# Kernel tuning notes

Hardware: AMD Instinct MI355X
Metric: run time of the kernel (lower is better)

## Reference

```python
import jax, jax.numpy as jnp
import numpy as np

WORD_TOTAL = 1_000_000
POS_TOTAL = 123
DIM = 50        # word embedding dim
DWPE = 5        # position embedding dim
C = 230         # conv filters (dimensionC)
WIN = 3         # conv window
REL = 53        # relationTotal
B = 1024        # bag size (number of sentences)
L = 128         # sentence length


def setup_inputs() -> dict:
    key = jax.random.key(0)
    ks = jax.random.split(key, 12)
    con = np.sqrt(6.0 / (C + REL))
    con1 = np.sqrt(6.0 / ((DWPE + DIM) * WIN))
    inp = {
        "sen": jax.random.randint(ks[0], (B, L), 0, WORD_TOTAL),
        "p1": jax.random.randint(ks[1], (B, L), 0, POS_TOTAL),
        "p2": jax.random.randint(ks[2], (B, L), 0, POS_TOTAL),
        "wordVec": jax.random.normal(ks[3], (WORD_TOTAL, DIM), jnp.float32) * 0.05,
        "posVec1": jax.random.normal(ks[4], (POS_TOTAL, DWPE), jnp.float32) * con1,
        "posVec2": jax.random.normal(ks[5], (POS_TOTAL, DWPE), jnp.float32) * con1,
        "Wv": jax.random.normal(ks[6], (WIN, DIM, C), jnp.float32) * 0.05,
        "Wp1": jax.random.normal(ks[7], (WIN, DWPE, C), jnp.float32) * 0.05,
        "Wp2": jax.random.normal(ks[8], (WIN, DWPE, C), jnp.float32) * 0.05,
        "bv": jnp.zeros((C,), jnp.float32),
        "bp1": jnp.zeros((C,), jnp.float32),
        "bp2": jnp.zeros((C,), jnp.float32),
        "attW": jax.random.normal(ks[9], (C, C), jnp.float32) * con,
        "MR": jax.random.normal(ks[10], (C, REL), jnp.float32) * 0.05,
        "MRb": jnp.zeros((REL,), jnp.float32),
        "rel": 7,
    }
    return inp


def _conv_full_width(emb, W):
    Lout = emb.shape[1] - WIN + 1
    wins = jnp.stack([emb[:, j:j + Lout, :] for j in range(WIN)], axis=0)
    return jnp.einsum('jbld,jdc->blc', wins, W)  # [B, Lout, C]


def reference(sen, p1, p2, wordVec, posVec1, posVec2, Wv, bv, Wp1, bp1, Wp2, bp2, attW, MR, MRb, rel):
    # ---- encode: per-sentence PCNN-style encoder, batched over the bag ----
    ev = wordVec[sen]   # [B, L, DIM]
    e1 = posVec1[p1]    # [B, L, DWPE]
    e2 = posVec2[p2]    # [B, L, DWPE]
    c = (_conv_full_width(ev, Wv) + bv
         + _conv_full_width(e1, Wp1) + bp1
         + _conv_full_width(e2, Wp2) + bp2)          # [B, Lout, C]
    cnn_output = jnp.tanh(jnp.max(c, axis=1))          # [B, C]
    # ---- selective attention over the bag (training=False: dropout identity) ----
    scores = (cnn_output @ attW) @ MR + MRb            # [B, REL]
    weight = jax.nn.softmax(scores[:, rel])            # [B] = exp/sum(exp)
    att_output = jnp.sum(weight[:, None] * cnn_output, axis=0)[None, :]  # [1, C]
    output = jax.nn.softmax(att_output @ MR + MRb)     # [1, REL]
    return (output, att_output, cnn_output, weight[:, None])
```

## Files before the change

kernel.cpp:

```cpp
#include <hip/hip_runtime.h>
#include <math.h>

#define CCH 230
#define REL 53
#define BAG 1024
#define SLEN 128
#define LOUT 126

typedef __bf16 bf16x8 __attribute__((ext_vector_type(8)));
typedef float f32x4 __attribute__((ext_vector_type(4)));

#define WS_BF_USHORTS (16 * 6 * 64 * 8)
#define WS_BSUM 24576
#define WS_V    24832
#define WS_SCORES 25088

__device__ __forceinline__ unsigned short f2bf(float f) {
    unsigned u = __builtin_bit_cast(unsigned, f);
    unsigned r = (u + 0x7fffu + ((u >> 16) & 1u)) >> 16;
    return (unsigned short)r;
}

__global__ void pa_kernel(const float* __restrict__ Wv, const float* __restrict__ Wp1,
                          const float* __restrict__ Wp2, const float* __restrict__ bv,
                          const float* __restrict__ bp1, const float* __restrict__ bp2,
                          const float* __restrict__ attW, const float* __restrict__ MR,
                          const int* __restrict__ relp, float* __restrict__ ws,
                          float* __restrict__ att_out) {
    if (blockIdx.x < 193) {
        int idx = blockIdx.x * 256 + threadIdx.x;
        if (idx < WS_BF_USHORTS) {
            int j = idx & 7;
            int lane = (idx >> 3) & 63;
            int q = idx >> 9;
            int ks = q % 6, ntile = q / 6;
            int n = ntile * 16 + (lane & 15);
            int k = ks * 32 + (lane >> 4) * 8 + j;
            float v = 0.f;
            if (k < 180 && n < CCH) {
                int jw = k / 60;
                int d = k - jw * 60;
                if (d < 50)      v = Wv[(jw * 50 + d) * CCH + n];
                else if (d < 55) v = Wp1[(jw * 5 + (d - 50)) * CCH + n];
                else             v = Wp2[(jw * 5 + (d - 55)) * CCH + n];
            }
            ((unsigned short*)ws)[idx] = f2bf(v);
        } else {
            int ch = idx - WS_BF_USHORTS;
            float v = 0.f;
            if (ch < CCH) { v = bv[ch] + bp1[ch] + bp2[ch]; att_out[ch] = 0.f; }
            ws[WS_BSUM + ch] = v;
        }
    } else {
        int i = (blockIdx.x - 193) * 4 + (threadIdx.x >> 6);
        int lane = threadIdx.x & 63;
        if (i < CCH) {
            int rel = *relp;
            float s = 0.f;
            for (int j = lane; j < CCH; j += 64) s += attW[i * CCH + j] * MR[j * REL + rel];
            for (int off = 32; off > 0; off >>= 1) s += __shfl_down(s, off, 64);
            if (lane == 0) ws[WS_V + i] = s;
        }
    }
}

__global__ __launch_bounds__(512, 4) void conv_kernel(
    const int* __restrict__ sen, const int* __restrict__ p1, const int* __restrict__ p2,
    const float* __restrict__ wordVec, const float* __restrict__ posVec1,
    const float* __restrict__ posVec2, const float* __restrict__ ws,
    const float* __restrict__ MRb, const int* __restrict__ relp,
    float* __restrict__ cnn_out, float* __restrict__ scores) {
    __shared__ __align__(16) unsigned short x_lds[132 * 60];
    __shared__ float s_red[8];
    const int b = blockIdx.x;
    const int tid = threadIdx.x;
    const int lane = tid & 63, w = tid >> 6;
    const int quad = lane >> 4, l16 = lane & 15;
    const unsigned short* wsu = (const unsigned short*)ws;

    bf16x8 bfrag[6][2];
    #pragma unroll
    for (int ks = 0; ks < 6; ++ks)
        #pragma unroll
        for (int nt = 0; nt < 2; ++nt) {
            int ntile = w * 2 + nt;
            bfrag[ks][nt] = *reinterpret_cast<const bf16x8*>(wsu + ((ntile * 6 + ks) * 64 + lane) * 8);
        }

    {
        int l = tid >> 2, t = tid & 3;
        int si = sen[b * SLEN + l];
        if (t < 3) {
            float v[16];
            const float* base = wordVec + si * 50 + t * 16;
            #pragma unroll
            for (int k2 = 0; k2 < 8; ++k2) {
                float2 f = *reinterpret_cast<const float2*>(base + 2 * k2);
                v[2 * k2] = f.x; v[2 * k2 + 1] = f.y;
            }
            ushort4* dst = reinterpret_cast<ushort4*>(x_lds + l * 60 + t * 16);
            #pragma unroll
            for (int q = 0; q < 4; ++q) {
                ushort4 o;
                o.x = f2bf(v[4 * q + 0]); o.y = f2bf(v[4 * q + 1]);
                o.z = f2bf(v[4 * q + 2]); o.w = f2bf(v[4 * q + 3]);
                dst[q] = o;
            }
        } else {
            float v[12];
            float2 wv = *reinterpret_cast<const float2*>(wordVec + si * 50 + 48);
            v[0] = wv.x; v[1] = wv.y;
            int i1 = p1[b * SLEN + l] * 5, i2 = p2[b * SLEN + l] * 5;
            #pragma unroll
            for (int j = 0; j < 5; ++j) { v[2 + j] = posVec1[i1 + j]; v[7 + j] = posVec2[i2 + j]; }
            ushort4* dst = reinterpret_cast<ushort4*>(x_lds + l * 60 + 48);
            #pragma unroll
            for (int q = 0; q < 3; ++q) {
                ushort4 o;
                o.x = f2bf(v[4 * q + 0]); o.y = f2bf(v[4 * q + 1]);
                o.z = f2bf(v[4 * q + 2]); o.w = f2bf(v[4 * q + 3]);
                dst[q] = o;
            }
        }
    }
    if (tid < 16) {
        int l = SLEN + (tid >> 2), t = tid & 3;
        ushort4 z; z.x = z.y = z.z = z.w = 0;
        ushort4* dst = reinterpret_cast<ushort4*>(x_lds + l * 60 + ((t < 3) ? t * 16 : 48));
        if (t < 3) { dst[0] = z; dst[1] = z; dst[2] = z; dst[3] = z; }
        else       { dst[0] = z; dst[1] = z; dst[2] = z; }
    }
    __syncthreads();

    f32x4 acc[8][2];
    #pragma unroll
    for (int mt = 0; mt < 8; ++mt)
        #pragma unroll
        for (int nt = 0; nt < 2; ++nt) acc[mt][nt] = (f32x4){0.f, 0.f, 0.f, 0.f};

    union AU { uint2 u2[2]; bf16x8 v; };

    #pragma unroll
    for (int ks = 0; ks < 6; ++ks) {
        int kg = ks * 4 + quad;
        #pragma unroll
        for (int mt = 0; mt < 8; ++mt) {
            int m = mt * 16 + l16;
            const uint2* ap = reinterpret_cast<const uint2*>(x_lds + m * 60 + kg * 8);
            AU a; a.u2[0] = ap[0]; a.u2[1] = ap[1];
            #pragma unroll
            for (int nt = 0; nt < 2; ++nt)
                acc[mt][nt] = __builtin_amdgcn_mfma_f32_16x16x32_bf16(a.v, bfrag[ks][nt], acc[mt][nt], 0, 0, 0);
        }
    }

    float vals[2];
    #pragma unroll
    for (int nt = 0; nt < 2; ++nt) {
        float mv = -3.0e38f;
        #pragma unroll
        for (int mt = 0; mt < 8; ++mt) {
            #pragma unroll
            for (int r = 0; r < 4; ++r) {
                int l = mt * 16 + quad * 4 + r;
                if (l < LOUT) mv = fmaxf(mv, acc[mt][nt][r]);
            }
        }
        mv = fmaxf(mv, __shfl_xor(mv, 16, 64));
        mv = fmaxf(mv, __shfl_xor(mv, 32, 64));
        int ch = w * 32 + nt * 16 + l16;
        float t = tanhf(mv + ws[WS_BSUM + ch]);
        vals[nt] = t;
        if (quad == 0 && ch < CCH) cnn_out[b * CCH + ch] = t;
    }

    float s = 0.f;
    if (quad == 0) {
        #pragma unroll
        for (int nt = 0; nt < 2; ++nt) {
            int ch = w * 32 + nt * 16 + l16;
            if (ch < CCH) s += vals[nt] * ws[WS_V + ch];
        }
    }
    for (int off = 32; off > 0; off >>= 1) s += __shfl_down(s, off, 64);
    if (lane == 0) s_red[w] = s;
    __syncthreads();
    if (tid == 0) {
        float t = MRb[*relp];
        #pragma unroll
        for (int i = 0; i < 8; ++i) t += s_red[i];
        scores[b] = t;
    }
}

__global__ void final1_kernel(const float* __restrict__ cnn, const float* __restrict__ scores,
                              float* __restrict__ att_out, float* __restrict__ w_out) {
    __shared__ float redm[4], reds[4];
    __shared__ float wloc[32];
    int tid = threadIdx.x, g = blockIdx.x;
    float s0[4];
    float mx = -3.0e38f;
    #pragma unroll
    for (int k = 0; k < 4; ++k) { s0[k] = scores[tid + 256 * k]; mx = fmaxf(mx, s0[k]); }
    #pragma unroll
    for (int off = 32; off > 0; off >>= 1) mx = fmaxf(mx, __shfl_xor(mx, off, 64));
    if ((tid & 63) == 0) redm[tid >> 6] = mx;
    __syncthreads();
    mx = fmaxf(fmaxf(redm[0], redm[1]), fmaxf(redm[2], redm[3]));
    float sum = 0.f;
    #pragma unroll
    for (int k = 0; k < 4; ++k) sum += expf(s0[k] - mx);
    #pragma unroll
    for (int off = 32; off > 0; off >>= 1) sum += __shfl_xor(sum, off, 64);
    if ((tid & 63) == 0) reds[tid >> 6] = sum;
    __syncthreads();
    sum = reds[0] + reds[1] + reds[2] + reds[3];

    int b0 = g * 32;
    if (tid < 32) {
        float w = expf(scores[b0 + tid] - mx) / sum;
        wloc[tid] = w;
        w_out[b0 + tid] = w;
    }
    __syncthreads();
    if (tid < CCH) {
        float a = 0.f;
        #pragma unroll 8
        for (int bb = 0; bb < 32; ++bb) a += wloc[bb] * cnn[(b0 + bb) * CCH + tid];
        atomicAdd(&att_out[tid], a);
    }
}

__global__ void final2_kernel(const float* __restrict__ att_in, const float* __restrict__ MR,
                              const float* __restrict__ MRb, float* __restrict__ out0) {
    __shared__ float MRs[CCH * REL];
    __shared__ float atts[CCH];
    __shared__ float lbuf[64];
    int tid = threadIdx.x;
    for (int i = tid; i < CCH * REL; i += 256) MRs[i] = MR[i];
    if (tid < CCH) atts[tid] = att_in[tid];
    __syncthreads();
    float t = 0.f;
    if (tid < REL) {
        t = MRb[tid];
        #pragma unroll 10
        for (int c = 0; c < CCH; ++c) t += atts[c] * MRs[c * REL + tid];
        lbuf[tid] = t;
    }
    __syncthreads();
    if (tid == 0) {
        float m2 = -3.0e38f;
        for (int i = 0; i < REL; ++i) m2 = fmaxf(m2, lbuf[i]);
        float s2 = 0.f;
        for (int i = 0; i < REL; ++i) s2 += expf(lbuf[i] - m2);
        lbuf[60] = m2; lbuf[61] = s2;
    }
    __syncthreads();
    if (tid < REL) out0[tid] = expf(t - lbuf[60]) / lbuf[61];
}

extern "C" void kernel_launch(void* const* d_in, const int* in_sizes, int n_in,
                              void* d_out, int out_size, void* d_ws, size_t ws_size,
                              hipStream_t stream) {
    const int* sen = (const int*)d_in[0];
    const int* p1  = (const int*)d_in[1];
    const int* p2  = (const int*)d_in[2];
    const float* wordVec = (const float*)d_in[3];
    const float* posVec1 = (const float*)d_in[4];
    const float* posVec2 = (const float*)d_in[5];
    const float* Wv  = (const float*)d_in[6];
    const float* Wp1 = (const float*)d_in[7];
    const float* Wp2 = (const float*)d_in[8];
    const float* bv  = (const float*)d_in[9];
    const float* bp1 = (const float*)d_in[10];
    const float* bp2 = (const float*)d_in[11];
    const float* attW = (const float*)d_in[12];
    const float* MR  = (const float*)d_in[13];
    const float* MRb = (const float*)d_in[14];
    const int* relp  = (const int*)d_in[15];

    float* ws = (float*)d_ws;
    float* out = (float*)d_out;
    float* out0    = out;
    float* att_out = out + REL;
    float* cnn_out = out + REL + CCH;
    float* w_out   = out + REL + CCH + BAG * CCH;

    hipLaunchKernelGGL(pa_kernel, dim3(193 + 58), dim3(256), 0, stream,
                       Wv, Wp1, Wp2, bv, bp1, bp2, attW, MR, relp, ws, att_out);
    hipLaunchKernelGGL(conv_kernel, dim3(BAG), dim3(512), 0, stream,
                       sen, p1, p2, wordVec, posVec1, posVec2, ws, MRb, relp,
                       cnn_out, ws + WS_SCORES);
    hipLaunchKernelGGL(final1_kernel, dim3(32), dim3(256), 0, stream,
                       cnn_out, ws + WS_SCORES, att_out, w_out);
    hipLaunchKernelGGL(final2_kernel, dim3(1), dim3(256), 0, stream,
                       att_out, MR, MRb, out0);
}
```

Before: 303.4 us.

## Fuse final kernels with last-block counter and atomically accumulate attention scores

Merges the two tail kernels into one: after each block adds its share into att_out, a global counter picks the last-arriving block to compute the relation logits and softmax. That block reads MR straight from global memory instead of staging it in LDS. The conv kernel now adds each wave's partial score into a pre-zeroed scores buffer with an atomic, dropping the LDS reduction and trailing barrier. MRb[rel] is no longer added because softmax is shift-invariant. This removes one kernel launch and some synchronisation, at the cost of atomics and a serial final stage in a single block.

```diff
diff --git a/kernel.cpp b/kernel.cpp
--- a/kernel.cpp
+++ b/kernel.cpp
@@ -14,6 +14,7 @@
 #define WS_BSUM 24576
 #define WS_V    24832
 #define WS_SCORES 25088
+#define WS_CNT  26112
 
 __device__ __forceinline__ unsigned short f2bf(float f) {
     unsigned u = __builtin_bit_cast(unsigned, f);
@@ -27,8 +28,9 @@
                           const float* __restrict__ attW, const float* __restrict__ MR,
                           const int* __restrict__ relp, float* __restrict__ ws,
                           float* __restrict__ att_out) {
-    if (blockIdx.x < 193) {
-        int idx = blockIdx.x * 256 + threadIdx.x;
+    int bid = blockIdx.x;
+    if (bid < 193) {
+        int idx = bid * 256 + threadIdx.x;
         if (idx < WS_BF_USHORTS) {
             int j = idx & 7;
             int lane = (idx >> 3) & 63;
@@ -49,10 +51,13 @@
             int ch = idx - WS_BF_USHORTS;
             float v = 0.f;
             if (ch < CCH) { v = bv[ch] + bp1[ch] + bp2[ch]; att_out[ch] = 0.f; }
+            if (ch == 240) *((unsigned int*)(ws + WS_CNT)) = 0u;
             ws[WS_BSUM + ch] = v;
         }
+    } else if (bid < 197) {
+        ws[WS_SCORES + (bid - 193) * 256 + threadIdx.x] = 0.f;
     } else {
-        int i = (blockIdx.x - 193) * 4 + (threadIdx.x >> 6);
+        int i = (bid - 197) * 4 + (threadIdx.x >> 6);
         int lane = threadIdx.x & 63;
         if (i < CCH) {
             int rel = *relp;
@@ -68,10 +73,8 @@
     const int* __restrict__ sen, const int* __restrict__ p1, const int* __restrict__ p2,
     const float* __restrict__ wordVec, const float* __restrict__ posVec1,
     const float* __restrict__ posVec2, const float* __restrict__ ws,
-    const float* __restrict__ MRb, const int* __restrict__ relp,
     float* __restrict__ cnn_out, float* __restrict__ scores) {
     __shared__ __align__(16) unsigned short x_lds[132 * 60];
-    __shared__ float s_red[8];
     const int b = blockIdx.x;
     const int tid = threadIdx.x;
     const int lane = tid & 63, w = tid >> 6;
@@ -183,21 +186,21 @@
         }
     }
     for (int off = 32; off > 0; off >>= 1) s += __shfl_down(s, off, 64);
-    if (lane == 0) s_red[w] = s;
-    __syncthreads();
-    if (tid == 0) {
-        float t = MRb[*relp];
-        #pragma unroll
-        for (int i = 0; i < 8; ++i) t += s_red[i];
-        scores[b] = t;
-    }
-}
-
-__global__ void final1_kernel(const float* __restrict__ cnn, const float* __restrict__ scores,
-                              float* __restrict__ att_out, float* __restrict__ w_out) {
+    if (lane == 0) atomicAdd(&scores[b], s);
+}
+
+__global__ __launch_bounds__(256) void final_kernel(
+    const float* __restrict__ cnn, const float* __restrict__ scores,
+    const float* __restrict__ MR, const float* __restrict__ MRb,
+    float* __restrict__ att_out, float* __restrict__ w_out,
+    float* __restrict__ out0, unsigned int* __restrict__ cnt) {
     __shared__ float redm[4], reds[4];
     __shared__ float wloc[32];
+    __shared__ float atts[CCH];
+    __shared__ float lbuf[64];
+    __shared__ int sdone;
     int tid = threadIdx.x, g = blockIdx.x;
+
     float s0[4];
     float mx = -3.0e38f;
     #pragma unroll
@@ -229,22 +232,22 @@
         for (int bb = 0; bb < 32; ++bb) a += wloc[bb] * cnn[(b0 + bb) * CCH + tid];
         atomicAdd(&att_out[tid], a);
     }
-}
-
-__global__ void final2_kernel(const float* __restrict__ att_in, const float* __restrict__ MR,
-                              const float* __restrict__ MRb, float* __restrict__ out0) {
-    __shared__ float MRs[CCH * REL];
-    __shared__ float atts[CCH];
-    __shared__ float lbuf[64];
-    int tid = threadIdx.x;
-    for (int i = tid; i < CCH * REL; i += 256) MRs[i] = MR[i];
-    if (tid < CCH) atts[tid] = att_in[tid];
+    __syncthreads();
+    if (tid == 0) {
+        __threadfence();
+        unsigned int old = atomicAdd(cnt, 1u);
+        sdone = (old == 31u);
+    }
+    __syncthreads();
+    if (!sdone) return;
+
+    if (tid < CCH) atts[tid] = atomicAdd(&att_out[tid], 0.0f);
     __syncthreads();
     float t = 0.f;
     if (tid < REL) {
         t = MRb[tid];
         #pragma unroll 10
-        for (int c = 0; c < CCH; ++c) t += atts[c] * MRs[c * REL + tid];
+        for (int c = 0; c < CCH; ++c) t += atts[c] * MR[c * REL + tid];
         lbuf[tid] = t;
     }
     __syncthreads();
@@ -286,13 +289,12 @@
     float* cnn_out = out + REL + CCH;
     float* w_out   = out + REL + CCH + BAG * CCH;
 
-    hipLaunchKernelGGL(pa_kernel, dim3(193 + 58), dim3(256), 0, stream,
+    hipLaunchKernelGGL(pa_kernel, dim3(255), dim3(256), 0, stream,
                        Wv, Wp1, Wp2, bv, bp1, bp2, attW, MR, relp, ws, att_out);
     hipLaunchKernelGGL(conv_kernel, dim3(BAG), dim3(512), 0, stream,
-                       sen, p1, p2, wordVec, posVec1, posVec2, ws, MRb, relp,
+                       sen, p1, p2, wordVec, posVec1, posVec2, ws,
                        cnn_out, ws + WS_SCORES);
-    hipLaunchKernelGGL(final1_kernel, dim3(32), dim3(256), 0, stream,
-                       cnn_out, ws + WS_SCORES, att_out, w_out);
-    hipLaunchKernelGGL(final2_kernel, dim3(1), dim3(256), 0, stream,
-                       att_out, MR, MRb, out0);
-}
+    hipLaunchKernelGGL(final_kernel, dim3(32), dim3(256), 0, stream,
+                       cnn_out, ws + WS_SCORES, MR, MRb, att_out, w_out, out0,
+                       (unsigned int*)(ws + WS_CNT));
+}
```

Measured after the change: 305.2 us. About the same (+0.6%).
